# Kernel optimization log

Measured on AMD Instinct MI355X. Metric: run time of the kernel, lower is better.

## Reference

```python
import jax, jax.numpy as jnp
import numpy as np

H = 8          # n_heads
LORA_SCALE = 1.0


def _lora(x, down, up):
    # nn.Linear convention: y = x @ W.T ; down:[r,in], up:[out,r]
    return (x @ down.T) @ up.T


def setup_inputs() -> dict:
    key = jax.random.key(0)
    ks = jax.random.split(key, 16)
    B, S, D, R = 4, 2048, 640, 4
    std = 1.0 / np.sqrt(D)
    inp = {
        "hidden_states": jax.random.normal(ks[0], (B, S, D), jnp.float32),
        "wq": jax.random.normal(ks[1], (D, D), jnp.float32) * std,
        "wk": jax.random.normal(ks[2], (D, D), jnp.float32) * std,
        "wv": jax.random.normal(ks[3], (D, D), jnp.float32) * std,
        "wo": jax.random.normal(ks[4], (D, D), jnp.float32) * std,
        "bo": jax.random.normal(ks[5], (D,), jnp.float32) * 0.02,
        "q_down": jax.random.normal(ks[6], (R, D), jnp.float32) * (1.0 / R),
        "q_up": jax.random.normal(ks[7], (D, R), jnp.float32) * 0.02,
        "k_down": jax.random.normal(ks[8], (R, D), jnp.float32) * (1.0 / R),
        "k_up": jax.random.normal(ks[9], (D, R), jnp.float32) * 0.02,
        "v_down": jax.random.normal(ks[10], (R, D), jnp.float32) * (1.0 / R),
        "v_up": jax.random.normal(ks[11], (D, R), jnp.float32) * 0.02,
        "o_down": jax.random.normal(ks[12], (R, D), jnp.float32) * (1.0 / R),
        "o_up": jax.random.normal(ks[13], (D, R), jnp.float32) * 0.02,
    }
    return inp


def reference(hidden_states, wq, wk, wv, wo, bo,
              q_down, q_up, k_down, k_up, v_down, v_up, o_down, o_up):
    B, S, D = hidden_states.shape
    hd = D // H
    sm_scale = 1.0 / np.sqrt(hd)

    x = hidden_states  # self-attention: encoder_hidden_states = hidden_states
    q = x @ wq.T + LORA_SCALE * _lora(x, q_down, q_up)
    k = x @ wk.T + LORA_SCALE * _lora(x, k_down, k_up)
    v = x @ wv.T + LORA_SCALE * _lora(x, v_down, v_up)

    # head_to_batch_dim: [B,S,D] -> [B,H,S,hd]
    q = q.reshape(B, S, H, hd).transpose(0, 2, 1, 3)
    k = k.reshape(B, S, H, hd).transpose(0, 2, 1, 3)
    v = v.reshape(B, S, H, hd).transpose(0, 2, 1, 3)

    # get_attention_scores: baddbmm(beta=0, alpha=1/sqrt(hd)) + softmax
    scores = jnp.einsum("bhqd,bhkd->bhqk", q, k) * sm_scale
    probs = jax.nn.softmax(scores, axis=-1)
    attn_out = jnp.einsum("bhqk,bhkd->bhqd", probs, v)

    # batch_to_head_dim: [B,H,S,hd] -> [B,S,D]
    attn_out = attn_out.transpose(0, 2, 1, 3).reshape(B, S, D)

    # out projection (with bias) + LoRA on the pre-projection hidden states
    out = attn_out @ wo.T + bo + LORA_SCALE * _lora(attn_out, o_down, o_up)
    # to_out[1] is dropout -> identity at eval
    return out
```

## Files before the change

kernel.cpp:

```cpp
#include <hip/hip_runtime.h>

typedef unsigned short u16;
typedef unsigned int u32;
typedef unsigned long long u64;

typedef __bf16 bf16x8 __attribute__((ext_vector_type(8)));
typedef float f32x4 __attribute__((ext_vector_type(4)));
typedef float f32x16 __attribute__((ext_vector_type(16)));

__device__ __forceinline__ float b2f(u16 u) {
    union { u32 i; float f; } c; c.i = ((u32)u) << 16; return c.f;
}
__device__ __forceinline__ u16 f2b(float f) {
    union { float f; u32 i; } c; c.f = f;
    u32 r = c.i + 0x7fffu + ((c.i >> 16) & 1u);
    return (u16)(r >> 16);
}
__device__ __forceinline__ u32 cvt_pk_bf16(float a, float b) {
    u32 r;
    asm("v_cvt_pk_bf16_f32 %0, %1, %2" : "=v"(r) : "v"(a), "v"(b));
    return r;
}
__device__ __forceinline__ float fexp2(float x) {
    float r;
    asm("v_exp_f32 %0, %1" : "=v"(r) : "v"(x));
    return r;
}

__device__ __forceinline__ f32x4 mfma16(bf16x8 a, bf16x8 b, f32x4 c) {
    return __builtin_amdgcn_mfma_f32_16x16x32_bf16(a, b, c, 0, 0, 0);
}
__device__ __forceinline__ f32x16 mfma32(bf16x8 a, bf16x8 b, f32x16 c) {
    return __builtin_amdgcn_mfma_f32_32x32x16_bf16(a, b, c, 0, 0, 0);
}

__device__ __forceinline__ void lds_cp16(const u16* gsrc, u16* ldst) {
    __builtin_amdgcn_global_load_lds(
        (const __attribute__((address_space(1))) u32*)gsrc,
        (__attribute__((address_space(3))) u32*)ldst, 16, 0, 0);
}

struct ConvJobs {
    const float* s[4];
    u16* d[4];
};

__global__ __launch_bounds__(256) void convert_w(ConvJobs J, u16* __restrict__ vt,
                                                 int do_pad) {
    int j = blockIdx.y;
    int idx = blockIdx.x * 256 + threadIdx.x;
    if (j < 4) {
        if (idx >= 102400) return;
        float4 v = ((const float4*)J.s[j])[idx];
        ushort4 o;
        o.x = f2b(v.x); o.y = f2b(v.y); o.z = f2b(v.z); o.w = f2b(v.w);
        ((ushort4*)J.d[j])[idx] = o;
    } else if (do_pad) {
        int q = idx * 4;
        int bh = q >> 15;
        int rem = q & 32767;
        int row = rem >> 11, col = rem & 2047;
        u16 val = (row == 0) ? (u16)0x3F80 : (u16)0;
        ushort4 o = make_ushort4(val, val, val, val);
        *(ushort4*)(vt + ((size_t)bh * 96 + 80 + row) * 2048 + col) = o;
    }
}

__global__ __launch_bounds__(256) void fuse_x(const float* __restrict__ x,
                                              const float* __restrict__ qd,
                                              const float* __restrict__ kd,
                                              const float* __restrict__ vd,
                                              u16* __restrict__ xb,
                                              float* __restrict__ T) {
    int m = blockIdx.x * 4 + (threadIdx.x >> 6);
    int lane = threadIdx.x & 63;
    const float* row = x + (size_t)m * 640;
    u16* orow = xb + (size_t)m * 640;
    float acc[12];
#pragma unroll
    for (int r = 0; r < 12; ++r) acc[r] = 0.f;
#pragma unroll
    for (int ii = 0; ii < 10; ++ii) {
        int i = lane + ii * 64;
        float a = row[i];
        orow[i] = f2b(a);
#pragma unroll
        for (int r = 0; r < 4; ++r) {
            acc[r]     += a * qd[r * 640 + i];
            acc[4 + r] += a * kd[r * 640 + i];
            acc[8 + r] += a * vd[r * 640 + i];
        }
    }
#pragma unroll
    for (int off = 32; off > 0; off >>= 1)
#pragma unroll
        for (int r = 0; r < 12; ++r) acc[r] += __shfl_xor(acc[r], off);
    if (lane == 0) {
#pragma unroll
        for (int p = 0; p < 3; ++p) {
            float4* t = (float4*)(T + ((size_t)p * 8192 + m) * 4);
            *t = make_float4(acc[p * 4], acc[p * 4 + 1], acc[p * 4 + 2], acc[p * 4 + 3]);
        }
    }
}

__global__ __launch_bounds__(256) void lora_down_o(const u16* __restrict__ A,
                                                   const float* __restrict__ dn,
                                                   float* __restrict__ T) {
    int m = blockIdx.x * 4 + (threadIdx.x >> 6);
    int lane = threadIdx.x & 63;
    const u16* arow = A + (size_t)m * 640;
    float a0 = 0.f, a1 = 0.f, a2 = 0.f, a3 = 0.f;
    for (int i = lane; i < 640; i += 64) {
        float a = b2f(arow[i]);
        a0 += a * dn[i];
        a1 += a * dn[640 + i];
        a2 += a * dn[1280 + i];
        a3 += a * dn[1920 + i];
    }
#pragma unroll
    for (int off = 32; off > 0; off >>= 1) {
        a0 += __shfl_xor(a0, off);
        a1 += __shfl_xor(a1, off);
        a2 += __shfl_xor(a2, off);
        a3 += __shfl_xor(a3, off);
    }
    if (lane == 0) {
        float4* t = (float4*)(T + (size_t)m * 4);
        *t = make_float4(a0, a1, a2, a3);
    }
}

struct QkvPtrs {
    const u16* W[3];
    const float* up[3];
    void* out[3];
    float scale[3];
    int mode[3];
};

__global__ __launch_bounds__(256) void gemm_bt(const u16* __restrict__ A, QkvPtrs P,
                                               const float* __restrict__ T,
                                               const float* __restrict__ bias) {
    int z = blockIdx.z;
    const u16* W = P.W[z];
    const float* up = P.up[z];
    const float scl = P.scale[z];
    const int md = P.mode[z];
    const float* Tz = T + (size_t)z * 8192 * 4;
    int m0 = blockIdx.x * 128, n0 = blockIdx.y * 128;
    int tid = threadIdx.x, lane = tid & 63, wid = tid >> 6;
    int g = lane >> 4, l15 = lane & 15;
    __shared__ __align__(16) u16 As[128 * 32];
    __shared__ __align__(16) u16 Bs[128 * 32];
    f32x4 acc[4][4] = {};
    int wm = (wid & 1) * 64, wn = (wid >> 1) * 64;

    for (int k0 = 0; k0 < 640; k0 += 32) {
        __syncthreads();
#pragma unroll
        for (int it = 0; it < 2; ++it) {
            int f = tid + it * 256;
            int r = f >> 2, c = f & 3;
            lds_cp16(A + (size_t)(m0 + r) * 640 + k0 + c * 8, As + f * 8);
            lds_cp16(W + (size_t)(n0 + r) * 640 + k0 + c * 8, Bs + f * 8);
        }
        __syncthreads();
        bf16x8 af[4], bfv[4];
#pragma unroll
        for (int t = 0; t < 4; ++t) {
            af[t] = *(const bf16x8*)(As + (wm + t * 16 + l15) * 32 + g * 8);
            bfv[t] = *(const bf16x8*)(Bs + (wn + t * 16 + l15) * 32 + g * 8);
        }
#pragma unroll
        for (int i = 0; i < 4; ++i)
#pragma unroll
            for (int j = 0; j < 4; ++j)
                acc[i][j] = mfma16(af[i], bfv[j], acc[i][j]);
    }

    float4 upv[4];
    float bv[4];
#pragma unroll
    for (int j = 0; j < 4; ++j) {
        int n = n0 + wn + j * 16 + l15;
        upv[j] = *(const float4*)(up + n * 4);
        bv[j] = (md == 1) ? bias[n] : 0.f;
    }
    float* outf = (float*)P.out[z];
    u16* outb = (u16*)P.out[z];
#pragma unroll
    for (int i = 0; i < 4; ++i) {
#pragma unroll
        for (int r = 0; r < 4; ++r) {
            int m = m0 + wm + i * 16 + g * 4 + r;
            const float4 tv = *(const float4*)(Tz + (size_t)m * 4);
#pragma unroll
            for (int j = 0; j < 4; ++j) {
                int n = n0 + wn + j * 16 + l15;
                float v = acc[i][j][r] + tv.x * upv[j].x + tv.y * upv[j].y +
                          tv.z * upv[j].z + tv.w * upv[j].w + bv[j];
                if (md == 1) {
                    outf[(size_t)m * 640 + n] = v;
                } else if (md == 0) {
                    int bb = m >> 11, s = m & 2047;
                    int h = n / 80, d = n - h * 80;
                    outb[(((size_t)bb * 8 + h) * 2048 + s) * 80 + d] = f2b(v * scl);
                } else {
                    int bb = m >> 11, s = m & 2047;
                    int h = n / 80, d = n - h * 80;
                    int sp = (s & ~12) | ((s & 4) << 1) | ((s & 8) >> 1);
                    outb[(((size_t)bb * 8 + h) * 96 + d) * 2048 + sp] = f2b(v);
                }
            }
        }
    }
}

__global__ __launch_bounds__(256) void transpose_v(const u16* __restrict__ Vin,
                                                   u16* __restrict__ Vout) {
    __shared__ u32 lds32[64 * 41];
    int bh = blockIdx.y;
    int s0 = blockIdx.x * 64;
    int tid = threadIdx.x;
    const u16* in = Vin + (size_t)bh * 2048 * 80;
    u16* out = Vout + (size_t)bh * 96 * 2048;

    for (int t = tid; t < 640; t += 256) {
        int s = t / 10, c = t - s * 10;
        uint4 v = *(const uint4*)(in + (size_t)(s0 + s) * 80 + c * 8);
        u32* p = lds32 + s * 41 + c * 4;
        p[0] = v.x; p[1] = v.y; p[2] = v.z; p[3] = v.w;
    }
    __syncthreads();
    for (int t = tid; t < 640; t += 256) {
        int d = t >> 3, c8 = t & 7;
        int dp = d >> 1, hi = d & 1;
        u16 vals[8];
#pragma unroll
        for (int j = 0; j < 8; ++j) {
            u32 w = lds32[(c8 * 8 + j) * 41 + dp];
            vals[j] = hi ? (u16)(w >> 16) : (u16)(w & 0xffff);
        }
        u16* dst = out + (size_t)d * 2048 + s0 + (c8 >> 1) * 16 + (c8 & 1) * 4;
        *(uint2*)dst = *(const uint2*)(vals);
        *(uint2*)(dst + 8) = *(const uint2*)(vals + 4);
    }
    for (int t = tid; t < 1024; t += 256) {
        int r = t >> 6, c = t & 63;
        out[(size_t)(80 + r) * 2048 + s0 + c] = (r == 0) ? 0x3F80 : 0;
    }
}

__global__ __launch_bounds__(512) void flash_attn(const u16* __restrict__ Q,
                                                  const u16* __restrict__ K,
                                                  const u16* __restrict__ Vt_g,
                                                  u16* __restrict__ O) {
    int bh = blockIdx.y;
    int q0 = blockIdx.x * 256;
    int tid = threadIdx.x;
    int lane = tid & 63, wid = tid >> 6, l31 = lane & 31, h2 = lane >> 5;
    const size_t base = (size_t)bh * 2048 * 80;
    const size_t vbase = (size_t)bh * 96 * 2048;

    __shared__ __align__(16) u16 lds[2 * 5632 + 2 * 7200];
    u16* Ks0 = lds;
    u16* Vt0 = lds + 11264;

    bf16x8 qf[5];
    {
        int qrow = q0 + wid * 32 + l31;
#pragma unroll
        for (int ks = 0; ks < 5; ++ks)
            qf[ks] = *(const bf16x8*)(Q + base + (size_t)qrow * 80 + ks * 16 + h2 * 8);
    }

    f32x16 oa[3] = {};
    const float C2 = 17.312340490667562f;

    auto stage = [&](int buf, int kt) {
#pragma unroll
        for (int it = 0; it < 4; ++it) {
            int c = tid + it * 512;
            if (c < 704) {
                int row = c / 11, col = c - row * 11;
                lds_cp16(K + base + (size_t)(kt + row) * 80 + col * 8,
                         Ks0 + buf * 5632 + c * 8);
            } else if (c < 1600) {
                int t = c - 704;
                int row = t / 9, col = t - row * 9;
                lds_cp16(Vt_g + vbase + (size_t)row * 2048 + kt + col * 8,
                         Vt0 + buf * 7200 + t * 8);
            }
        }
    };

    stage(0, 0);
    __syncthreads();

    for (int i = 0; i < 32; ++i) {
        int cur = i & 1;
        if (i < 31) stage(cur ^ 1, (i + 1) * 64);

        const u16* ks = Ks0 + cur * 5632;
        const u16* vt = Vt0 + cur * 7200;

#pragma unroll
        for (int kk2 = 0; kk2 < 2; ++kk2) {
            f32x16 s = {};
            __builtin_amdgcn_s_setprio(1);
#pragma unroll
            for (int ks5 = 0; ks5 < 5; ++ks5) {
                bf16x8 kf = *(const bf16x8*)(ks + (kk2 * 32 + l31) * 88 + ks5 * 16 + h2 * 8);
                s = mfma32(kf, qf[ks5], s);
            }
            __builtin_amdgcn_s_setprio(0);
            u32 d[8];
#pragma unroll
            for (int j = 0; j < 8; ++j)
                d[j] = cvt_pk_bf16(fexp2(s[2 * j] - C2), fexp2(s[2 * j + 1] - C2));
            __builtin_amdgcn_s_setprio(1);
#pragma unroll
            for (int sl = 0; sl < 2; ++sl) {
                union { u32 w[4]; bf16x8 v; } pa;
                pa.w[0] = d[4 * sl + 0];
                pa.w[1] = d[4 * sl + 1];
                pa.w[2] = d[4 * sl + 2];
                pa.w[3] = d[4 * sl + 3];
#pragma unroll
                for (int nt = 0; nt < 3; ++nt) {
                    bf16x8 vf = *(const bf16x8*)(vt + (nt * 32 + l31) * 72 +
                                                 kk2 * 32 + sl * 16 + h2 * 8);
                    oa[nt] = mfma32(pa.v, vf, oa[nt]);
                }
            }
            __builtin_amdgcn_s_setprio(0);
        }
        __syncthreads();
    }

    int b = bh >> 3, h = bh & 7;
    float inv[16];
#pragma unroll
    for (int reg = 0; reg < 16; ++reg)
        inv[reg] = 1.f / __shfl(oa[2][reg], (lane & 32) + 16, 64);
#pragma unroll
    for (int nt = 0; nt < 3; ++nt) {
        int vd = nt * 32 + l31;
        if (vd < 80) {
#pragma unroll
            for (int reg = 0; reg < 16; ++reg) {
                int q = q0 + wid * 32 + (reg & 3) + 8 * (reg >> 2) + 4 * h2;
                O[((size_t)(b * 2048 + q)) * 640 + h * 80 + vd] = f2b(oa[nt][reg] * inv[reg]);
            }
        }
    }
}

extern "C" void kernel_launch(void* const* d_in, const int* in_sizes, int n_in,
                              void* d_out, int out_size, void* d_ws, size_t ws_size,
                              hipStream_t stream) {
    const float* x      = (const float*)d_in[0];
    const float* wq     = (const float*)d_in[1];
    const float* wk     = (const float*)d_in[2];
    const float* wv     = (const float*)d_in[3];
    const float* wo     = (const float*)d_in[4];
    const float* bo     = (const float*)d_in[5];
    const float* q_down = (const float*)d_in[6];
    const float* q_up   = (const float*)d_in[7];
    const float* k_down = (const float*)d_in[8];
    const float* k_up   = (const float*)d_in[9];
    const float* v_down = (const float*)d_in[10];
    const float* v_up   = (const float*)d_in[11];
    const float* o_down = (const float*)d_in[12];
    const float* o_up   = (const float*)d_in[13];

    char* ws = (char*)d_ws;
    u16* xb    = (u16*)(ws);
    u16* wbv   = (u16*)(ws + 10485760);
    u16* wbq   = (u16*)(ws + 11304960);
    u16* wbk   = (u16*)(ws + 12124160);
    u16* wbo   = (u16*)(ws + 12943360);
    u16* q_ws  = (u16*)(ws + 13762560);
    u16* k_ws  = (u16*)(ws + 24248320);
    u16* v_ws  = (u16*)(ws + 34734080);
    u16* attn  = (u16*)(ws + 45219840);
    float* Tq  = (float*)(ws + 55705600);
    float* To  = (float*)(ws + 56098816);

    const size_t vt_off = 56360960;
    const size_t vt_need = vt_off + 12582912 + 16384;
    const bool direct_vt = (ws_size >= vt_need);
    u16* vT_ws = direct_vt ? (u16*)(ws + vt_off)
                           : (u16*)(ws);

    ConvJobs cj;
    cj.s[0] = wq; cj.d[0] = wbq;
    cj.s[1] = wk; cj.d[1] = wbk;
    cj.s[2] = wv; cj.d[2] = wbv;
    cj.s[3] = wo; cj.d[3] = wbo;
    convert_w<<<dim3(1024, 5), 256, 0, stream>>>(cj, vT_ws, direct_vt ? 1 : 0);

    fuse_x<<<2048, 256, 0, stream>>>(x, q_down, k_down, v_down, xb, Tq);

    QkvPtrs pq;
    pq.W[0] = wbq; pq.W[1] = wbk; pq.W[2] = wbv;
    pq.up[0] = q_up; pq.up[1] = k_up; pq.up[2] = v_up;
    pq.out[0] = q_ws; pq.out[1] = k_ws;
    pq.out[2] = direct_vt ? (void*)vT_ws : (void*)v_ws;
    pq.scale[0] = 0.11180339887498949f * 1.4426950408889634f;
    pq.scale[1] = 1.0f;
    pq.scale[2] = 1.0f;
    pq.mode[0] = 0; pq.mode[1] = 0; pq.mode[2] = direct_vt ? 2 : 0;
    gemm_bt<<<dim3(64, 5, 3), 256, 0, stream>>>(xb, pq, Tq, bo);

    if (!direct_vt)
        transpose_v<<<dim3(32, 32), 256, 0, stream>>>(v_ws, vT_ws);

    flash_attn<<<dim3(8, 32), 512, 0, stream>>>(q_ws, k_ws, vT_ws, attn);

    lora_down_o<<<2048, 256, 0, stream>>>(attn, o_down, To);

    QkvPtrs po;
    po.W[0] = wbo; po.W[1] = wbo; po.W[2] = wbo;
    po.up[0] = o_up; po.up[1] = o_up; po.up[2] = o_up;
    po.out[0] = d_out; po.out[1] = d_out; po.out[2] = d_out;
    po.scale[0] = 1.0f; po.scale[1] = 1.0f; po.scale[2] = 1.0f;
    po.mode[0] = 1; po.mode[1] = 1; po.mode[2] = 1;
    gemm_bt<<<dim3(64, 5, 1), 256, 0, stream>>>(attn, po, To, bo);
}
```

Measured before the change: 241.8 us.

## Double-buffer GEMM LDS tiles and keep Q/K in token-major layout

New measurement: 248.9 us. 1.03x slower.

```diff
diff --git a/kernel.cpp b/kernel.cpp
--- a/kernel.cpp
+++ b/kernel.cpp
@@ -151,32 +151,44 @@
     int m0 = blockIdx.x * 128, n0 = blockIdx.y * 128;
     int tid = threadIdx.x, lane = tid & 63, wid = tid >> 6;
     int g = lane >> 4, l15 = lane & 15;
-    __shared__ __align__(16) u16 As[128 * 32];
-    __shared__ __align__(16) u16 Bs[128 * 32];
+    __shared__ __align__(16) u16 As[2][4096];
+    __shared__ __align__(16) u16 Bs[2][4096];
     f32x4 acc[4][4] = {};
     int wm = (wid & 1) * 64, wn = (wid >> 1) * 64;
 
-    for (int k0 = 0; k0 < 640; k0 += 32) {
-        __syncthreads();
-#pragma unroll
-        for (int it = 0; it < 2; ++it) {
-            int f = tid + it * 256;
-            int r = f >> 2, c = f & 3;
-            lds_cp16(A + (size_t)(m0 + r) * 640 + k0 + c * 8, As + f * 8);
-            lds_cp16(W + (size_t)(n0 + r) * 640 + k0 + c * 8, Bs + f * 8);
-        }
-        __syncthreads();
+    int r0 = tid >> 2, cb = (tid & 3) * 8;
+    const u16* pA = A + (size_t)(m0 + r0) * 640 + cb;
+    const u16* pB = W + (size_t)(n0 + r0) * 640 + cb;
+    u16* dA = &As[0][0] + tid * 8;
+    u16* dB = &Bs[0][0] + tid * 8;
+
+    auto stage = [&](int buf, int k0) {
+        lds_cp16(pA + k0, dA + buf * 4096);
+        lds_cp16(pA + 40960 + k0, dA + buf * 4096 + 2048);
+        lds_cp16(pB + k0, dB + buf * 4096);
+        lds_cp16(pB + 40960 + k0, dB + buf * 4096 + 2048);
+    };
+
+    stage(0, 0);
+    __syncthreads();
+
+    for (int t = 0; t < 20; ++t) {
+        int cur = t & 1;
+        if (t < 19) stage(cur ^ 1, (t + 1) * 32);
+        const u16* as = &As[0][0] + cur * 4096;
+        const u16* bs = &Bs[0][0] + cur * 4096;
         bf16x8 af[4], bfv[4];
 #pragma unroll
-        for (int t = 0; t < 4; ++t) {
-            af[t] = *(const bf16x8*)(As + (wm + t * 16 + l15) * 32 + g * 8);
-            bfv[t] = *(const bf16x8*)(Bs + (wn + t * 16 + l15) * 32 + g * 8);
+        for (int q4 = 0; q4 < 4; ++q4) {
+            af[q4]  = *(const bf16x8*)(as + (wm + q4 * 16 + l15) * 32 + g * 8);
+            bfv[q4] = *(const bf16x8*)(bs + (wn + q4 * 16 + l15) * 32 + g * 8);
         }
 #pragma unroll
         for (int i = 0; i < 4; ++i)
 #pragma unroll
             for (int j = 0; j < 4; ++j)
                 acc[i][j] = mfma16(af[i], bfv[j], acc[i][j]);
+        __syncthreads();
     }
 
     float4 upv[4];
@@ -200,7 +212,9 @@
                 int n = n0 + wn + j * 16 + l15;
                 float v = acc[i][j][r] + tv.x * upv[j].x + tv.y * upv[j].y +
                           tv.z * upv[j].z + tv.w * upv[j].w + bv[j];
-                if (md == 1) {
+                if (md == 3) {
+                    outb[(size_t)m * 640 + n] = f2b(v * scl);
+                } else if (md == 1) {
                     outf[(size_t)m * 640 + n] = v;
                 } else if (md == 0) {
                     int bb = m >> 11, s = m & 2047;
@@ -260,7 +274,8 @@
     int q0 = blockIdx.x * 256;
     int tid = threadIdx.x;
     int lane = tid & 63, wid = tid >> 6, l31 = lane & 31, h2 = lane >> 5;
-    const size_t base = (size_t)bh * 2048 * 80;
+    int b = bh >> 3, h = bh & 7;
+    const size_t tbase = (size_t)b * 2048 * 640 + (size_t)h * 80;
     const size_t vbase = (size_t)bh * 96 * 2048;
 
     __shared__ __align__(16) u16 lds[2 * 5632 + 2 * 7200];
@@ -272,7 +287,7 @@
         int qrow = q0 + wid * 32 + l31;
 #pragma unroll
         for (int ks = 0; ks < 5; ++ks)
-            qf[ks] = *(const bf16x8*)(Q + base + (size_t)qrow * 80 + ks * 16 + h2 * 8);
+            qf[ks] = *(const bf16x8*)(Q + tbase + (size_t)qrow * 640 + ks * 16 + h2 * 8);
     }
 
     f32x16 oa[3] = {};
@@ -284,7 +299,7 @@
             int c = tid + it * 512;
             if (c < 704) {
                 int row = c / 11, col = c - row * 11;
-                lds_cp16(K + base + (size_t)(kt + row) * 80 + col * 8,
+                lds_cp16(K + tbase + (size_t)(kt + row) * 640 + col * 8,
                          Ks0 + buf * 5632 + c * 8);
             } else if (c < 1600) {
                 int t = c - 704;
@@ -339,7 +354,6 @@
         __syncthreads();
     }
 
-    int b = bh >> 3, h = bh & 7;
     float inv[16];
 #pragma unroll
     for (int reg = 0; reg < 16; ++reg)
@@ -411,7 +425,7 @@
     pq.scale[0] = 0.11180339887498949f * 1.4426950408889634f;
     pq.scale[1] = 1.0f;
     pq.scale[2] = 1.0f;
-    pq.mode[0] = 0; pq.mode[1] = 0; pq.mode[2] = direct_vt ? 2 : 0;
+    pq.mode[0] = 3; pq.mode[1] = 3; pq.mode[2] = direct_vt ? 2 : 0;
     gemm_bt<<<dim3(64, 5, 3), 256, 0, stream>>>(xb, pq, Tq, bo);
 
     if (!direct_vt)
```
